# Performance work log

Hardware: AMD Instinct MI355X
Metric: run time of the kernel (lower is better)

Reference implementation:

```python
import jax, jax.numpy as jnp
import numpy as np

EMBED_DIM = 768
NUM_HEADS = 12
HEAD_DIM = EMBED_DIM // NUM_HEADS
B, T = 2, 2048


def setup_inputs() -> dict:
    key = jax.random.key(0)
    ks = jax.random.split(key, 11)
    s = 1.0 / np.sqrt(EMBED_DIM)
    return {
        "query": jax.random.normal(ks[0], (B, T, EMBED_DIM), jnp.float32),
        "key_in": jax.random.normal(ks[1], (B, T, EMBED_DIM), jnp.float32),
        "value": jax.random.normal(ks[2], (B, T, EMBED_DIM), jnp.float32),
        "Wq": jax.random.uniform(ks[3], (EMBED_DIM, EMBED_DIM), jnp.float32, -s, s),
        "bq": jnp.zeros((EMBED_DIM,), jnp.float32),
        "Wk": jax.random.uniform(ks[4], (EMBED_DIM, EMBED_DIM), jnp.float32, -s, s),
        "bk": jnp.zeros((EMBED_DIM,), jnp.float32),
        "Wv": jax.random.uniform(ks[5], (EMBED_DIM, EMBED_DIM), jnp.float32, -s, s),
        "bv": jnp.zeros((EMBED_DIM,), jnp.float32),
        "Wo": jax.random.uniform(ks[6], (EMBED_DIM, EMBED_DIM), jnp.float32, -s, s),
        "bo": jnp.zeros((EMBED_DIM,), jnp.float32),
    }


def reference(query, key_in, value, Wq, bq, Wk, bk, Wv, bv, Wo, bo):
    b, t, _ = query.shape

    def split_heads(x):  # [B,T,E] -> [B,H,T,Dh]
        return x.reshape(b, t, NUM_HEADS, HEAD_DIM).transpose(0, 2, 1, 3)

    Q = split_heads(query @ Wq + bq)
    K = split_heads(key_in @ Wk + bk)
    V = split_heads(value @ Wv + bv)

    scores = jnp.einsum("bhqd,bhkd->bhqk", Q, K) / np.sqrt(HEAD_DIM).astype(np.float32)
    attn = jax.nn.softmax(scores, axis=-1)
    out = jnp.einsum("bhqk,bhkd->bhqd", attn, V)  # [B,H,T,Dh]
    out = out.transpose(0, 2, 1, 3).reshape(b, t, EMBED_DIM)
    return out @ Wo + bo
```

## Files before the change

### kernel.cpp

```cpp
#include <hip/hip_runtime.h>
#include <math.h>

typedef __attribute__((ext_vector_type(4))) float  floatx4;
typedef __attribute__((ext_vector_type(16))) float f32x16;
typedef __attribute__((ext_vector_type(8))) short  short8;
typedef __attribute__((ext_vector_type(4))) short  short4v;
typedef __attribute__((ext_vector_type(8))) __bf16 bf16x8;
typedef __attribute__((ext_vector_type(4))) unsigned int uint4v;

#define E_DIM 768
#define T_DIM 2048
#define N_B   2
#define N_H   12
#define H_D   64
#define M_TOT 4096

#define Q_SCALE 0.1803368801111204f

#if __has_builtin(__builtin_amdgcn_exp2f)
#define EXP2F(x) __builtin_amdgcn_exp2f(x)
#else
#define EXP2F(x) exp2f(x)
#endif
#if __has_builtin(__builtin_amdgcn_rcpf)
#define RCPF(x) __builtin_amdgcn_rcpf(x)
#else
#define RCPF(x) (1.0f / (x))
#endif

__device__ __forceinline__ unsigned short f32_to_bf16(float f) {
  unsigned int u = __float_as_uint(f);
  u += 0x7fffu + ((u >> 16) & 1u);
  return (unsigned short)(u >> 16);
}

__device__ __forceinline__ void lds_barrier() {
  asm volatile("s_waitcnt lgkmcnt(0)\n\ts_barrier" ::: "memory");
}

__device__ __forceinline__ void gload_lds16(const unsigned short* g, unsigned short* l) {
  __builtin_amdgcn_global_load_lds(
      (const __attribute__((address_space(1))) unsigned int*)(const void*)g,
      (__attribute__((address_space(3))) unsigned int*)(void*)l, 16, 0, 0);
}

__device__ __forceinline__ unsigned int cvtpk_bf16(float lo, float hi) {
  unsigned int r;
  asm("v_cvt_pk_bf16_f32 %0, %1, %2" : "=v"(r) : "v"(lo), "v"(hi));
  return r;
}

__device__ __forceinline__ void perml32_swap(unsigned int& a, unsigned int& b) {
  asm volatile("v_permlane32_swap_b32 %0, %1" : "+v"(a), "+v"(b));
}

__global__ __launch_bounds__(256) void convert_x(const float* __restrict__ q,
                                                 const float* __restrict__ k,
                                                 const float* __restrict__ v,
                                                 unsigned short* __restrict__ Xb) {
  const int z = blockIdx.y;
  const float* src = (z == 0) ? q : (z == 1) ? k : v;
  size_t idx = ((size_t)blockIdx.x * 256 + threadIdx.x) * 4;
  float4 val = *reinterpret_cast<const float4*>(&src[idx]);
  short4v o;
  o[0] = (short)f32_to_bf16(val.x);
  o[1] = (short)f32_to_bf16(val.y);
  o[2] = (short)f32_to_bf16(val.z);
  o[3] = (short)f32_to_bf16(val.w);
  *reinterpret_cast<short4v*>(&Xb[(size_t)z * M_TOT * E_DIM + idx]) = o;
}

__global__ __launch_bounds__(256) void transpose_w4(const float* __restrict__ W0,
                                                    const float* __restrict__ W1,
                                                    const float* __restrict__ W2,
                                                    const float* __restrict__ W3,
                                                    unsigned short* __restrict__ Wt) {
  __shared__ float tile[32][33];
  const int z = blockIdx.z;
  const float* W = (z == 0) ? W0 : (z == 1) ? W1 : (z == 2) ? W2 : W3;
  unsigned short* dst = Wt + (size_t)z * E_DIM * E_DIM;
  int k0 = blockIdx.x * 32, n0 = blockIdx.y * 32;
  int tx = threadIdx.x & 31, ty = threadIdx.x >> 5;
  for (int i = 0; i < 4; i++)
    tile[ty + i * 8][tx] = W[(size_t)(k0 + ty + i * 8) * E_DIM + n0 + tx];
  __syncthreads();
  for (int i = 0; i < 4; i++)
    dst[(size_t)(n0 + ty + i * 8) * E_DIM + k0 + tx] = f32_to_bf16(tile[tx][ty + i * 8]);
}

__global__ __launch_bounds__(256) void gemm_qkv(const unsigned short* __restrict__ Xb,
                                                const unsigned short* __restrict__ WtAll,
                                                const float* __restrict__ bq,
                                                const float* __restrict__ bk,
                                                const float* __restrict__ bv,
                                                unsigned short* __restrict__ outQKV) {
  __shared__ unsigned short As[128 * 32];
  __shared__ unsigned short Bs[128 * 32];

  const int z = blockIdx.z;
  const unsigned short* A = Xb + (size_t)z * M_TOT * E_DIM;
  const float* bias = (z == 0) ? bq : (z == 1) ? bk : bv;
  const unsigned short* W = WtAll + (size_t)z * E_DIM * E_DIM;
  unsigned short* out = outQKV + (size_t)z * M_TOT * E_DIM;
  const float scale = (z == 0) ? Q_SCALE : 1.0f;

  const int tid = threadIdx.x;
  const int lane = tid & 63, wv = tid >> 6;
  const int m15 = lane & 15, quad = lane >> 4;
  const int wm = (wv & 1) * 64, wn = (wv >> 1) * 64;
  const int m0 = blockIdx.x * 128, n0 = blockIdx.y * 128;

  floatx4 acc[4][4] = {};
  const int srow = lane >> 2, scol = (lane & 3) * 8;

  for (int k0 = 0; k0 < E_DIM; k0 += 32) {
    for (int cc = 0; cc < 2; cc++) {
      int c = wv * 2 + cc;
      gload_lds16(&A[(size_t)(m0 + c * 16 + srow) * E_DIM + k0 + scol], &As[c * 512]);
      gload_lds16(&W[(size_t)(n0 + c * 16 + srow) * E_DIM + k0 + scol], &Bs[c * 512]);
    }
    __syncthreads();
    bf16x8 af[4], bfr[4];
    for (int i = 0; i < 4; i++)
      af[i] = *reinterpret_cast<const bf16x8*>(&As[(wm + i * 16 + m15) * 32 + quad * 8]);
    for (int j = 0; j < 4; j++)
      bfr[j] = *reinterpret_cast<const bf16x8*>(&Bs[(wn + j * 16 + m15) * 32 + quad * 8]);
    for (int i = 0; i < 4; i++)
      for (int j = 0; j < 4; j++)
        acc[i][j] = __builtin_amdgcn_mfma_f32_16x16x32_bf16(af[i], bfr[j], acc[i][j], 0, 0, 0);
    __syncthreads();
  }

  for (int i = 0; i < 4; i++)
    for (int j = 0; j < 4; j++) {
      int gn = n0 + wn + j * 16 + m15;
      int h = gn >> 6, d = gn & 63;
      float bso = bias[gn];
      for (int r = 0; r < 4; r++) {
        int gm = m0 + wm + i * 16 + quad * 4 + r;
        int bb = gm >> 11, tt = gm & 2047;
        float v = (acc[i][j][r] + bso) * scale;
        out[(((size_t)bb * N_H + h) * T_DIM + tt) * H_D + d] = f32_to_bf16(v);
      }
    }
}

__global__ __launch_bounds__(256) void transpose_v(const unsigned short* __restrict__ Vg_all,
                                                   unsigned short* __restrict__ VT) {
  __shared__ unsigned short tile[64 * 72];
  const int t0 = blockIdx.x * 64, h = blockIdx.y, bb = blockIdx.z;
  const unsigned short* Vg = Vg_all + (((size_t)bb * N_H + h) * T_DIM) * H_D;
  unsigned short* VTh = VT + (((size_t)bb * N_H + h) * H_D) * T_DIM;
  const int tid = threadIdx.x;
  const int tloc = tid & 63, d0 = (tid >> 6) * 16;

  short8 r0 = *reinterpret_cast<const short8*>(&Vg[(size_t)(t0 + tloc) * H_D + d0]);
  short8 r1 = *reinterpret_cast<const short8*>(&Vg[(size_t)(t0 + tloc) * H_D + d0 + 8]);
#pragma unroll
  for (int j = 0; j < 8; j++) {
    tile[(d0 + j) * 72 + tloc] = (unsigned short)r0[j];
    tile[(d0 + 8 + j) * 72 + tloc] = (unsigned short)r1[j];
  }
  __syncthreads();
  const int d = tid >> 2, ts = (tid & 3) * 16;
  short8 w0 = *reinterpret_cast<const short8*>(&tile[d * 72 + ts]);
  short8 w1 = *reinterpret_cast<const short8*>(&tile[d * 72 + ts + 8]);
  *reinterpret_cast<short8*>(&VTh[(size_t)d * T_DIM + t0 + ts]) = w0;
  *reinterpret_cast<short8*>(&VTh[(size_t)d * T_DIM + t0 + ts + 8]) = w1;
}

__global__ __launch_bounds__(128) void attn(const unsigned short* __restrict__ QKV,
                                            const unsigned short* __restrict__ VT,
                                            unsigned short* __restrict__ ctx) {
  __shared__ unsigned short Ks[2][64 * 64];
  __shared__ unsigned short Vs[2][64 * 64];

  const int qt = blockIdx.x, h = blockIdx.y, bb = blockIdx.z;
  const size_t headoff = (((size_t)bb * N_H + h) * T_DIM) * H_D;
  const unsigned short* Qg = QKV + headoff;
  const unsigned short* Kg = QKV + (size_t)M_TOT * E_DIM + headoff;
  const unsigned short* VTg = VT + (((size_t)bb * N_H + h) * H_D) * T_DIM;

  const int tid = threadIdx.x;
  const int lane = tid & 63, wv = tid >> 6;
  const int l31 = lane & 31, hi = lane >> 5, l7 = lane & 7;
  const int q0 = qt * 64 + wv * 32;

  const int srow = lane >> 3;
  const int sslot = (lane & 7) ^ srow;
  const unsigned short* gK = Kg + (size_t)srow * H_D + sslot * 8;
  const unsigned short* gV = VTg + (size_t)srow * T_DIM + sslot * 8;

  bf16x8 aq[4];
#pragma unroll
  for (int c = 0; c < 4; c++)
    aq[c] = *reinterpret_cast<const bf16x8*>(&Qg[(size_t)(q0 + l31) * H_D + c * 16 + hi * 8]);

#pragma unroll
  for (int i = 0; i < 8; i++) {
    if (wv == 0) gload_lds16(gK + (size_t)(i * 8) * H_D, &Ks[0][i * 512]);
    else         gload_lds16(gV + (size_t)(i * 8) * T_DIM, &Vs[0][i * 512]);
  }
#pragma unroll
  for (int i = 0; i < 8; i++) {
    if (wv == 0) gload_lds16(gK + (size_t)(64 + i * 8) * H_D, &Ks[1][i * 512]);
    else         gload_lds16(gV + (size_t)(i * 8) * T_DIM + 64, &Vs[1][i * 512]);
  }
  asm volatile("s_waitcnt vmcnt(0)" ::: "memory");
  lds_barrier();

  f32x16 o0 = {}, o1 = {};
  float lacc = 0.f;

  for (int kt = 0; kt < 32; ++kt) {
    const unsigned short* kb = Ks[kt & 1];
    const unsigned short* vb = Vs[kt & 1];

    f32x16 s0 = {}, s1 = {};
#pragma unroll
    for (int c = 0; c < 4; c++) {
      const int slot = ((c << 1) | hi) ^ l7;
      bf16x8 k0 = *reinterpret_cast<const bf16x8*>(&kb[l31 * 64 + slot * 8]);
      bf16x8 k1 = *reinterpret_cast<const bf16x8*>(&kb[(32 + l31) * 64 + slot * 8]);
      s0 = __builtin_amdgcn_mfma_f32_32x32x16_bf16(k0, aq[c], s0, 0, 0, 0);
      s1 = __builtin_amdgcn_mfma_f32_32x32x16_bf16(k1, aq[c], s1, 0, 0, 0);
    }

#pragma unroll
    for (int i = 0; i < 16; i++) { s0[i] = EXP2F(s0[i]); s1[i] = EXP2F(s1[i]); }
    float ps = 0.f;
#pragma unroll
    for (int i = 0; i < 16; i++) ps += s0[i] + s1[i];
    lacc += ps;

    bf16x8 pa0[2], pa1[2];
#pragma unroll
    for (int cc = 0; cc < 2; cc++) {
      {
        unsigned int x0 = cvtpk_bf16(s0[8 * cc + 0], s0[8 * cc + 1]);
        unsigned int x1 = cvtpk_bf16(s0[8 * cc + 2], s0[8 * cc + 3]);
        unsigned int y0 = cvtpk_bf16(s0[8 * cc + 4], s0[8 * cc + 5]);
        unsigned int y1 = cvtpk_bf16(s0[8 * cc + 6], s0[8 * cc + 7]);
        perml32_swap(x0, y0);
        perml32_swap(x1, y1);
        uint4v u; u[0] = x0; u[1] = x1; u[2] = y0; u[3] = y1;
        pa0[cc] = __builtin_bit_cast(bf16x8, u);
      }
      {
        unsigned int x0 = cvtpk_bf16(s1[8 * cc + 0], s1[8 * cc + 1]);
        unsigned int x1 = cvtpk_bf16(s1[8 * cc + 2], s1[8 * cc + 3]);
        unsigned int y0 = cvtpk_bf16(s1[8 * cc + 4], s1[8 * cc + 5]);
        unsigned int y1 = cvtpk_bf16(s1[8 * cc + 6], s1[8 * cc + 7]);
        perml32_swap(x0, y0);
        perml32_swap(x1, y1);
        uint4v u; u[0] = x0; u[1] = x1; u[2] = y0; u[3] = y1;
        pa1[cc] = __builtin_bit_cast(bf16x8, u);
      }
    }

#pragma unroll
    for (int cc = 0; cc < 2; cc++) {
      const int sl0 = ((cc << 1) | hi) ^ l7;
      const int sl1 = (4 + (cc << 1) + hi) ^ l7;
      bf16x8 v00 = *reinterpret_cast<const bf16x8*>(&vb[l31 * 64 + sl0 * 8]);
      bf16x8 v01 = *reinterpret_cast<const bf16x8*>(&vb[(32 + l31) * 64 + sl0 * 8]);
      bf16x8 v10 = *reinterpret_cast<const bf16x8*>(&vb[l31 * 64 + sl1 * 8]);
      bf16x8 v11 = *reinterpret_cast<const bf16x8*>(&vb[(32 + l31) * 64 + sl1 * 8]);
      o0 = __builtin_amdgcn_mfma_f32_32x32x16_bf16(pa0[cc], v00, o0, 0, 0, 0);
      o1 = __builtin_amdgcn_mfma_f32_32x32x16_bf16(pa0[cc], v01, o1, 0, 0, 0);
      o0 = __builtin_amdgcn_mfma_f32_32x32x16_bf16(pa1[cc], v10, o0, 0, 0, 0);
      o1 = __builtin_amdgcn_mfma_f32_32x32x16_bf16(pa1[cc], v11, o1, 0, 0, 0);
    }

    if (kt == 31) break;
    lds_barrier();
    if (kt < 30) {
      const int nt = kt + 2;
#pragma unroll
      for (int i = 0; i < 8; i++) {
        if (wv == 0) gload_lds16(gK + (size_t)(nt * 64 + i * 8) * H_D, &Ks[kt & 1][i * 512]);
        else         gload_lds16(gV + (size_t)(i * 8) * T_DIM + nt * 64, &Vs[kt & 1][i * 512]);
      }
      asm volatile("s_waitcnt vmcnt(8)" ::: "memory");
    } else {
      asm volatile("s_waitcnt vmcnt(0)" ::: "memory");
    }
    lds_barrier();
  }

  float ltot = lacc + __shfl_xor(lacc, 32, 64);
  float rl = RCPF(ltot);
  const size_t obase = ((size_t)bb * T_DIM + q0) * E_DIM + (size_t)h * H_D;
#pragma unroll
  for (int r = 0; r < 16; r++) {
    const int qrow = (r & 3) + 8 * (r >> 2) + 4 * hi;
    float rq = __shfl(rl, qrow, 64);
    ctx[obase + (size_t)qrow * E_DIM + l31]      = f32_to_bf16(o0[r] * rq);
    ctx[obase + (size_t)qrow * E_DIM + 32 + l31] = f32_to_bf16(o1[r] * rq);
  }
}

__global__ __launch_bounds__(256) void gemm_out(const unsigned short* __restrict__ Actx,
                                                const unsigned short* __restrict__ Wt,
                                                const float* __restrict__ bias,
                                                float* __restrict__ out) {
  __shared__ unsigned short As[64 * 32];
  __shared__ unsigned short Bs[128 * 32];

  const int tid = threadIdx.x;
  const int lane = tid & 63, wv = tid >> 6;
  const int m15 = lane & 15, quad = lane >> 4;
  const int wm = (wv & 1) * 32, wn = (wv >> 1) * 64;
  const int m0 = blockIdx.x * 64, n0 = blockIdx.y * 128;

  floatx4 acc[2][4] = {};
  const int srow = lane >> 2, scol = (lane & 3) * 8;

  for (int k0 = 0; k0 < E_DIM; k0 += 32) {
    gload_lds16(&Actx[(size_t)(m0 + wv * 16 + srow) * E_DIM + k0 + scol], &As[wv * 512]);
    for (int cc = 0; cc < 2; cc++) {
      int c = wv * 2 + cc;
      gload_lds16(&Wt[(size_t)(n0 + c * 16 + srow) * E_DIM + k0 + scol], &Bs[c * 512]);
    }
    __syncthreads();
    bf16x8 af[2], bfr[4];
    for (int i = 0; i < 2; i++)
      af[i] = *reinterpret_cast<const bf16x8*>(&As[(wm + i * 16 + m15) * 32 + quad * 8]);
    for (int j = 0; j < 4; j++)
      bfr[j] = *reinterpret_cast<const bf16x8*>(&Bs[(wn + j * 16 + m15) * 32 + quad * 8]);
    for (int i = 0; i < 2; i++)
      for (int j = 0; j < 4; j++)
        acc[i][j] = __builtin_amdgcn_mfma_f32_16x16x32_bf16(af[i], bfr[j], acc[i][j], 0, 0, 0);
    __syncthreads();
  }

  for (int i = 0; i < 2; i++)
    for (int j = 0; j < 4; j++) {
      int gn = n0 + wn + j * 16 + m15;
      float bso = bias[gn];
      for (int r = 0; r < 4; r++) {
        int gm = m0 + wm + i * 16 + quad * 4 + r;
        out[(size_t)gm * E_DIM + gn] = acc[i][j][r] + bso;
      }
    }
}

extern "C" void kernel_launch(void* const* d_in, const int* in_sizes, int n_in,
                              void* d_out, int out_size, void* d_ws, size_t ws_size,
                              hipStream_t stream) {
  const float* query  = (const float*)d_in[0];
  const float* key_in = (const float*)d_in[1];
  const float* value  = (const float*)d_in[2];
  const float* Wq = (const float*)d_in[3];
  const float* bq = (const float*)d_in[4];
  const float* Wk = (const float*)d_in[5];
  const float* bk = (const float*)d_in[6];
  const float* Wv = (const float*)d_in[7];
  const float* bv = (const float*)d_in[8];
  const float* Wo = (const float*)d_in[9];
  const float* bo = (const float*)d_in[10];
  float* out = (float*)d_out;

  unsigned short* ws  = (unsigned short*)d_ws;
  unsigned short* Wt  = ws;
  unsigned short* Xb  = Wt + (size_t)4 * E_DIM * E_DIM;
  unsigned short* QKV = Xb + (size_t)3 * M_TOT * E_DIM;
  unsigned short* VT  = QKV + (size_t)3 * M_TOT * E_DIM;
  unsigned short* ctx = VT + (size_t)N_B * N_H * H_D * T_DIM;

  dim3 tb(256);
  convert_x<<<dim3(M_TOT * E_DIM / 1024, 3), tb, 0, stream>>>(query, key_in, value, Xb);
  transpose_w4<<<dim3(24, 24, 4), tb, 0, stream>>>(Wq, Wk, Wv, Wo, Wt);

  gemm_qkv<<<dim3(32, 6, 3), tb, 0, stream>>>(Xb, Wt, bq, bk, bv, QKV);
  transpose_v<<<dim3(32, 12, 2), tb, 0, stream>>>(QKV + (size_t)2 * M_TOT * E_DIM, VT);
  attn<<<dim3(32, 12, 2), dim3(128), 0, stream>>>(QKV, VT, ctx);
  gemm_out<<<dim3(64, 6), tb, 0, stream>>>(ctx, Wt + (size_t)3 * E_DIM * E_DIM, bo, out);
  (void)in_sizes; (void)n_in; (void)out_size; (void)ws_size;
}
```

Measured before the change: 205.3 us.

## Software-pipeline attention loop so QK of next tile overlaps PV of previous

```diff
diff --git a/kernel.cpp b/kernel.cpp
--- a/kernel.cpp
+++ b/kernel.cpp
@@ -201,22 +201,19 @@
     if (wv == 0) gload_lds16(gK + (size_t)(i * 8) * H_D, &Ks[0][i * 512]);
     else         gload_lds16(gV + (size_t)(i * 8) * T_DIM, &Vs[0][i * 512]);
   }
-#pragma unroll
-  for (int i = 0; i < 8; i++) {
-    if (wv == 0) gload_lds16(gK + (size_t)(64 + i * 8) * H_D, &Ks[1][i * 512]);
-    else         gload_lds16(gV + (size_t)(i * 8) * T_DIM + 64, &Vs[1][i * 512]);
+  if (wv == 0) {
+#pragma unroll
+    for (int i = 0; i < 8; i++)
+      gload_lds16(gK + (size_t)(64 + i * 8) * H_D, &Ks[1][i * 512]);
   }
   asm volatile("s_waitcnt vmcnt(0)" ::: "memory");
   lds_barrier();
 
   f32x16 o0 = {}, o1 = {};
   float lacc = 0.f;
-
-  for (int kt = 0; kt < 32; ++kt) {
-    const unsigned short* kb = Ks[kt & 1];
-    const unsigned short* vb = Vs[kt & 1];
-
-    f32x16 s0 = {}, s1 = {};
+  bf16x8 pa0[2], pa1[2];
+
+  auto QK = [&](const unsigned short* kb, f32x16& s0, f32x16& s1) {
 #pragma unroll
     for (int c = 0; c < 4; c++) {
       const int slot = ((c << 1) | hi) ^ l7;
@@ -225,15 +222,32 @@
       s0 = __builtin_amdgcn_mfma_f32_32x32x16_bf16(k0, aq[c], s0, 0, 0, 0);
       s1 = __builtin_amdgcn_mfma_f32_32x32x16_bf16(k1, aq[c], s1, 0, 0, 0);
     }
-
+  };
+  auto PV = [&](const unsigned short* vb) {
+#pragma unroll
+    for (int cc = 0; cc < 2; cc++) {
+      const int sl0 = ((cc << 1) | hi) ^ l7;
+      const int sl1 = (4 + (cc << 1) + hi) ^ l7;
+      bf16x8 v00 = *reinterpret_cast<const bf16x8*>(&vb[l31 * 64 + sl0 * 8]);
+      bf16x8 v01 = *reinterpret_cast<const bf16x8*>(&vb[(32 + l31) * 64 + sl0 * 8]);
+      bf16x8 v10 = *reinterpret_cast<const bf16x8*>(&vb[l31 * 64 + sl1 * 8]);
+      bf16x8 v11 = *reinterpret_cast<const bf16x8*>(&vb[(32 + l31) * 64 + sl1 * 8]);
+      o0 = __builtin_amdgcn_mfma_f32_32x32x16_bf16(pa0[cc], v00, o0, 0, 0, 0);
+      o1 = __builtin_amdgcn_mfma_f32_32x32x16_bf16(pa0[cc], v01, o1, 0, 0, 0);
+      o0 = __builtin_amdgcn_mfma_f32_32x32x16_bf16(pa1[cc], v10, o0, 0, 0, 0);
+      o1 = __builtin_amdgcn_mfma_f32_32x32x16_bf16(pa1[cc], v11, o1, 0, 0, 0);
+    }
+  };
+  auto PACK = [&](f32x16& s0, f32x16& s1) {
 #pragma unroll
     for (int i = 0; i < 16; i++) { s0[i] = EXP2F(s0[i]); s1[i] = EXP2F(s1[i]); }
-    float ps = 0.f;
-#pragma unroll
-    for (int i = 0; i < 16; i++) ps += s0[i] + s1[i];
-    lacc += ps;
-
-    bf16x8 pa0[2], pa1[2];
+    float a0 = 0.f, a1 = 0.f, a2 = 0.f, a3 = 0.f;
+#pragma unroll
+    for (int i = 0; i < 16; i += 4) {
+      a0 += s0[i]; a1 += s0[i + 1]; a2 += s0[i + 2]; a3 += s0[i + 3];
+      a0 += s1[i]; a1 += s1[i + 1]; a2 += s1[i + 2]; a3 += s1[i + 3];
+    }
+    lacc += (a0 + a1) + (a2 + a3);
 #pragma unroll
     for (int cc = 0; cc < 2; cc++) {
       {
@@ -257,35 +271,60 @@
         pa1[cc] = __builtin_bit_cast(bf16x8, u);
       }
     }
-
-#pragma unroll
-    for (int cc = 0; cc < 2; cc++) {
-      const int sl0 = ((cc << 1) | hi) ^ l7;
-      const int sl1 = (4 + (cc << 1) + hi) ^ l7;
-      bf16x8 v00 = *reinterpret_cast<const bf16x8*>(&vb[l31 * 64 + sl0 * 8]);
-      bf16x8 v01 = *reinterpret_cast<const bf16x8*>(&vb[(32 + l31) * 64 + sl0 * 8]);
-      bf16x8 v10 = *reinterpret_cast<const bf16x8*>(&vb[l31 * 64 + sl1 * 8]);
-      bf16x8 v11 = *reinterpret_cast<const bf16x8*>(&vb[(32 + l31) * 64 + sl1 * 8]);
-      o0 = __builtin_amdgcn_mfma_f32_32x32x16_bf16(pa0[cc], v00, o0, 0, 0, 0);
-      o1 = __builtin_amdgcn_mfma_f32_32x32x16_bf16(pa0[cc], v01, o1, 0, 0, 0);
-      o0 = __builtin_amdgcn_mfma_f32_32x32x16_bf16(pa1[cc], v10, o0, 0, 0, 0);
-      o1 = __builtin_amdgcn_mfma_f32_32x32x16_bf16(pa1[cc], v11, o1, 0, 0, 0);
-    }
-
-    if (kt == 31) break;
+  };
+
+  {
+    f32x16 s0 = {}, s1 = {};
+    __builtin_amdgcn_s_setprio(1);
+    QK(Ks[0], s0, s1);
+    __builtin_amdgcn_s_setprio(0);
     lds_barrier();
-    if (kt < 30) {
-      const int nt = kt + 2;
-#pragma unroll
-      for (int i = 0; i < 8; i++) {
-        if (wv == 0) gload_lds16(gK + (size_t)(nt * 64 + i * 8) * H_D, &Ks[kt & 1][i * 512]);
-        else         gload_lds16(gV + (size_t)(i * 8) * T_DIM + nt * 64, &Vs[kt & 1][i * 512]);
+#pragma unroll
+    for (int i = 0; i < 8; i++) {
+      if (wv == 0) gload_lds16(gK + (size_t)(128 + i * 8) * H_D, &Ks[0][i * 512]);
+      else         gload_lds16(gV + (size_t)(i * 8) * T_DIM + 64, &Vs[1][i * 512]);
+    }
+    PACK(s0, s1);
+    asm volatile("s_waitcnt vmcnt(8)" ::: "memory");
+    lds_barrier();
+  }
+
+  for (int kt = 1; kt <= 30; ++kt) {
+    f32x16 s0 = {}, s1 = {};
+    __builtin_amdgcn_s_setprio(1);
+    QK(Ks[kt & 1], s0, s1);
+    PV(Vs[(kt - 1) & 1]);
+    __builtin_amdgcn_s_setprio(0);
+    lds_barrier();
+    if (wv == 0) {
+      if (kt < 30) {
+        const int nt = kt + 2;
+#pragma unroll
+        for (int i = 0; i < 8; i++)
+          gload_lds16(gK + (size_t)(nt * 64 + i * 8) * H_D, &Ks[kt & 1][i * 512]);
       }
-      asm volatile("s_waitcnt vmcnt(8)" ::: "memory");
     } else {
-      asm volatile("s_waitcnt vmcnt(0)" ::: "memory");
-    }
+      const int nt = kt + 1;
+#pragma unroll
+      for (int i = 0; i < 8; i++)
+        gload_lds16(gV + (size_t)(i * 8) * T_DIM + nt * 64, &Vs[nt & 1][i * 512]);
+    }
+    PACK(s0, s1);
+    if (kt == 30) asm volatile("s_waitcnt vmcnt(0)" ::: "memory");
+    else          asm volatile("s_waitcnt vmcnt(8)" ::: "memory");
     lds_barrier();
+  }
+
+  {
+    f32x16 s0 = {}, s1 = {};
+    __builtin_amdgcn_s_setprio(1);
+    QK(Ks[1], s0, s1);
+    PV(Vs[0]);
+    __builtin_amdgcn_s_setprio(0);
+    PACK(s0, s1);
+    __builtin_amdgcn_s_setprio(1);
+    PV(Vs[1]);
+    __builtin_amdgcn_s_setprio(0);
   }
 
   float ltot = lacc + __shfl_xor(lacc, 32, 64);
```

Measured after the change: 194.6 us (median of 2 runs). 5.2% less time.
